# Kernel tuning notes

Hardware: AMD Instinct MI355X
Metric: run time of the kernel (lower is better)

## Reference

```python
import jax, jax.numpy as jnp
import numpy as np

NUM_BINS = 128  # 32 mid-band bins + 96 bottom-band bins
LN_EPS = 1e-5


def _mlp_scores(desc, W1, b1, g1, be1, W2, b2, Ws, bs):
    # Linear -> LayerNorm -> SiLU -> Linear -> score head
    h = desc @ W1 + b1
    mu = h.mean(-1, keepdims=True)
    var = h.var(-1, keepdims=True)
    h = (h - mu) * jax.lax.rsqrt(var + LN_EPS) * g1 + be1
    h = h * jax.nn.sigmoid(h)  # SiLU
    feat = h @ W2 + b2
    scores = (feat @ Ws + bs)[..., 0]  # [B, N]
    return scores


def _grid_ids(kpts, H, W):
    x = kpts[..., 0]
    y = kpts[..., 1]
    mid = (y > 0.2 * H) & (y <= 0.5 * H)
    btm = y > 0.5 * H
    mgx = jnp.clip((x / W * 8).astype(jnp.int32), 0, 7)
    mgy = jnp.clip(((y - 0.2 * H) / (0.3 * H) * 4).astype(jnp.int32), 0, 3)
    bgx = jnp.clip((x / W * 16).astype(jnp.int32), 0, 15)
    bgy = jnp.clip(((y - 0.5 * H) / (0.5 * H) * 6).astype(jnp.int32), 0, 5)
    gid = jnp.where(btm, 32 + bgy * 16 + bgx, jnp.where(mid, mgy * 8 + mgx, -1))
    return gid  # [B, N], -1 = not in any grid band


def _select_one(scores, gid, top_k):
    # strict-'>' loop in the original), then compact + top-k fallback.
    N = scores.shape[0]
    valid = gid >= 0
    seg = jnp.where(valid, gid, NUM_BINS)  # dump invalid pts in dummy bin
    binmax = jax.ops.segment_max(scores, seg, num_segments=NUM_BINS + 1)
    is_win = valid & (scores == binmax[seg])
    winner_idx = jax.ops.segment_min(
        jnp.where(is_win, jnp.arange(N), N), seg, num_segments=NUM_BINS + 1
    )[:NUM_BINS]  # N = empty bin sentinel
    bin_valid = winner_idx < N
    # stable sort: non-empty bins first, preserving bin order
    order = jnp.argsort((~bin_valid).astype(jnp.int32))
    winners = winner_idx[order]  # [NUM_BINS], trailing sentinels
    num_sel = jnp.sum(bin_valid)
    # mask out already-selected winners, top-k fallback on the rest
    win_mask = jnp.zeros(N, bool).at[jnp.where(bin_valid, winner_idx, N)].set(True, mode='drop')
    rem = jnp.where(win_mask, -1e10, scores)
    _, extra = jax.lax.top_k(rem, top_k)
    j = jnp.arange(top_k)
    sel = jnp.where(
        j < num_sel,
        winners[jnp.clip(j, 0, NUM_BINS - 1)],
        extra[jnp.clip(j - num_sel, 0, top_k - 1)],
    )
    return sel  # [top_k]


def setup_inputs() -> dict:
    key = jax.random.key(0)
    ks = jax.random.split(key, 4)
    B, N, IN, OUT = 8, 50000, 256, 128
    H, W = 376, 1241
    kpts = jax.random.uniform(ks[0], (B, N, 2), jnp.float32) * jnp.array([W, H], jnp.float32)
    desc = jax.random.normal(ks[1], (B, N, IN), jnp.float32)
    kw = jax.random.split(ks[2], 3)
    W1 = 0.01 * jax.random.normal(kw[0], (IN, 256), jnp.float32)
    b1 = jnp.zeros((256,), jnp.float32)
    g1 = jnp.ones((256,), jnp.float32)
    be1 = jnp.zeros((256,), jnp.float32)
    W2 = 0.01 * jax.random.normal(kw[1], (256, OUT), jnp.float32)
    b2 = jnp.zeros((OUT,), jnp.float32)
    Ws = 0.001 * jax.random.normal(kw[2], (OUT, 1), jnp.float32)
    bs = jnp.zeros((1,), jnp.float32)
    return {"kpts": kpts, "desc": desc, "H": H, "W": W, "top_k": 128,
            "W1": W1, "b1": b1, "g1": g1, "be1": be1,
            "W2": W2, "b2": b2, "Ws": Ws, "bs": bs}


def reference(kpts, desc, H, W, top_k, W1, b1, g1, be1, W2, b2, Ws, bs):
    scores = _mlp_scores(desc, W1, b1, g1, be1, W2, b2, Ws, bs)  # [B,N]
    gid = _grid_ids(kpts, H, W)  # [B,N]
    indices = jax.vmap(lambda s, g: _select_one(s, g, top_k))(scores, gid)  # [B,top_k]
    final_feat = jnp.take_along_axis(desc, indices[:, :, None], axis=1)  # [B,top_k,256]
    final_kpts = jnp.take_along_axis(kpts, indices[:, :, None], axis=1)  # [B,top_k,2]
    return final_feat, final_kpts, indices
```

## Files before the change

### kernel.cpp

```cpp
#include <hip/hip_runtime.h>

#define THREADS 256

typedef short bf16x8 __attribute__((ext_vector_type(8)));
typedef float f32x4 __attribute__((ext_vector_type(4)));

__device__ __forceinline__ unsigned short f2bf(float x) {
    unsigned u = __float_as_uint(x);
    unsigned r = u + 0x7FFFu + ((u >> 16) & 1u);
    return (unsigned short)(r >> 16);
}
__device__ __forceinline__ float bf2f(unsigned short h) {
    return __uint_as_float(((unsigned)h) << 16);
}
__device__ __forceinline__ unsigned score_key(float s) {
    unsigned u = __float_as_uint(s);
    return (u & 0x80000000u) ? ~u : (u | 0x80000000u);
}

__global__ void prep_kernel(const float* __restrict__ W2, const float* __restrict__ b2,
                            const float* __restrict__ Ws, const float* __restrict__ bs,
                            float* __restrict__ v, int OUT) {
    int j = threadIdx.x;
    float acc = 0.f;
    for (int o = 0; o < OUT; ++o) acc += W2[j * OUT + o] * Ws[o];
    v[j] = acc;
    if (j == 0) {
        float c = bs[0];
        for (int o = 0; o < OUT; ++o) c += b2[o] * Ws[o];
        v[256] = c;
    }
}

__global__ void prep_w1frag(const float* __restrict__ W1, uint4* __restrict__ wfrag) {
    const int s = blockIdx.x * 256 + threadIdx.x;
    const int rem = s & 2047;
    const int kt = s >> 11;
    const int c = rem >> 6;
    const int lane = rem & 63;
    const int h = c >> 4;
    const int nt = c & 15;
    const int col = nt * 16 + (lane & 15);
    const int kb = kt * 32 + (lane >> 4) * 8;
    unsigned pk[4];
#pragma unroll
    for (int q = 0; q < 4; ++q) {
        float x0 = W1[(size_t)(kb + 2 * q) * 256 + col];
        float x1 = W1[(size_t)(kb + 2 * q + 1) * 256 + col];
        unsigned short a0, a1;
        if (h == 0) { a0 = f2bf(x0); a1 = f2bf(x1); }
        else {
            a0 = f2bf(x0 - bf2f(f2bf(x0)));
            a1 = f2bf(x1 - bf2f(f2bf(x1)));
        }
        pk[q] = (unsigned)a0 | ((unsigned)a1 << 16);
    }
    wfrag[s] = make_uint4(pk[0], pk[1], pk[2], pk[3]);
}

__global__ void init_bins(unsigned long long* __restrict__ bins, int n) {
    int i = blockIdx.x * blockDim.x + threadIdx.x;
    if (i < n) bins[i] = 0ULL;
}

__global__ __launch_bounds__(256, 2) void score_kernel(
    const float* __restrict__ desc, const float* __restrict__ kpts,
    const uint4* __restrict__ wfrag,
    const float* __restrict__ b1, const float* __restrict__ g1, const float* __restrict__ be1,
    const int* __restrict__ Hp, const int* __restrict__ Wp,
    const float* __restrict__ v,
    float* __restrict__ scores, unsigned long long* __restrict__ bins,
    int N, int total)
{
    __shared__ uint4 AhS[8 * 64];
    __shared__ uint4 AlS[8 * 64];
    __shared__ uint4 BS[32 * 64];
    __shared__ float b1L[256], g1L[256], beL[256], vL[256];
    __shared__ float sumsL[128][2];
    __shared__ float ctermS;

    const int t = threadIdx.x;
    const int lane = t & 63;
    const int w = t >> 6;
    const int wm = w & 1, wn = w >> 1;
    const int row0 = blockIdx.x * 128;
    const int l15 = lane & 15, q4 = lane >> 4, h5 = lane >> 5;

    b1L[t] = b1[t]; g1L[t] = g1[t]; beL[t] = be1[t]; vL[t] = v[t];
    if (t == 0) ctermS = v[256];

    f32x4 acc[4][8];
#pragma unroll
    for (int m = 0; m < 4; ++m)
#pragma unroll
        for (int n = 0; n < 8; ++n) acc[m][n] = (f32x4){0.f, 0.f, 0.f, 0.f};

    const int argp = 2 * w + h5;
    const int arow = row0 + argp * 16 + l15;
    const int arowc = min(arow, total - 1);
    const int kgbit = q4 & 1;

    for (int kt = 0; kt < 8; ++kt) {
        __syncthreads();
        {
            uint4 btmp[8];
            const uint4* bsrc = wfrag + (size_t)kt * 2048 + t;
#pragma unroll
            for (int j = 0; j < 8; ++j) btmp[j] = bsrc[j * 256];
#pragma unroll
            for (int j = 0; j < 8; ++j) BS[j * 256 + t] = btmp[j];
        }
#pragma unroll
        for (int i = 0; i < 2; ++i) {
            const int kg = kgbit + 2 * i;
            const float* gp = desc + (size_t)arowc * 256 + kt * 32 + kg * 8;
            float4 f0 = *(const float4*)gp;
            float4 f1 = *(const float4*)(gp + 4);
            float f[8] = {f0.x, f0.y, f0.z, f0.w, f1.x, f1.y, f1.z, f1.w};
            unsigned hs[4], ls[4];
#pragma unroll
            for (int q = 0; q < 4; ++q) {
                unsigned short h0 = f2bf(f[2 * q]), h1 = f2bf(f[2 * q + 1]);
                unsigned short o0 = f2bf(f[2 * q] - bf2f(h0));
                unsigned short o1 = f2bf(f[2 * q + 1] - bf2f(h1));
                hs[q] = (unsigned)h0 | ((unsigned)h1 << 16);
                ls[q] = (unsigned)o0 | ((unsigned)o1 << 16);
            }
            const int slot = argp * 64 + kg * 16 + l15;
            AhS[slot] = make_uint4(hs[0], hs[1], hs[2], hs[3]);
            AlS[slot] = make_uint4(ls[0], ls[1], ls[2], ls[3]);
        }
        __syncthreads();
        bf16x8 ah[4], al[4];
#pragma unroll
        for (int m = 0; m < 4; ++m) {
            ah[m] = *(const bf16x8*)&AhS[(wm * 4 + m) * 64 + lane];
            al[m] = *(const bf16x8*)&AlS[(wm * 4 + m) * 64 + lane];
        }
#pragma unroll
        for (int n = 0; n < 8; ++n) {
            const int nt = wn * 8 + n;
            bf16x8 bh = *(const bf16x8*)&BS[nt * 64 + lane];
            bf16x8 bl = *(const bf16x8*)&BS[(16 + nt) * 64 + lane];
#pragma unroll
            for (int m = 0; m < 4; ++m) {
                acc[m][n] = __builtin_amdgcn_mfma_f32_16x16x32_bf16(ah[m], bh, acc[m][n], 0, 0, 0);
                acc[m][n] = __builtin_amdgcn_mfma_f32_16x16x32_bf16(ah[m], bl, acc[m][n], 0, 0, 0);
                acc[m][n] = __builtin_amdgcn_mfma_f32_16x16x32_bf16(al[m], bh, acc[m][n], 0, 0, 0);
                acc[m][n] = __builtin_amdgcn_mfma_f32_16x16x32_bf16(al[m], bl, acc[m][n], 0, 0, 0);
            }
        }
    }

    float bpart = 0.f;
#pragma unroll
    for (int n = 0; n < 8; ++n) bpart += b1L[wn * 128 + n * 16 + l15];

    float mu[4][4], rs[4][4];
#pragma unroll
    for (int m = 0; m < 4; ++m)
#pragma unroll
        for (int r = 0; r < 4; ++r) {
            float x = bpart;
#pragma unroll
            for (int n = 0; n < 8; ++n) x += acc[m][n][r];
#pragma unroll
            for (int mask = 1; mask <= 8; mask <<= 1) x += __shfl_xor(x, mask);
            if (l15 == 0) sumsL[wm * 64 + m * 16 + q4 * 4 + r][wn] = x;
        }
    __syncthreads();
#pragma unroll
    for (int m = 0; m < 4; ++m)
#pragma unroll
        for (int r = 0; r < 4; ++r) {
            const int rl = wm * 64 + m * 16 + q4 * 4 + r;
            mu[m][r] = (sumsL[rl][0] + sumsL[rl][1]) * (1.f / 256.f);
        }
    __syncthreads();
#pragma unroll
    for (int m = 0; m < 4; ++m)
#pragma unroll
        for (int r = 0; r < 4; ++r) {
            float x = 0.f;
#pragma unroll
            for (int n = 0; n < 8; ++n) {
                const float hv = acc[m][n][r] + b1L[wn * 128 + n * 16 + l15] - mu[m][r];
                x = fmaf(hv, hv, x);
            }
#pragma unroll
            for (int mask = 1; mask <= 8; mask <<= 1) x += __shfl_xor(x, mask);
            if (l15 == 0) sumsL[wm * 64 + m * 16 + q4 * 4 + r][wn] = x;
        }
    __syncthreads();
#pragma unroll
    for (int m = 0; m < 4; ++m)
#pragma unroll
        for (int r = 0; r < 4; ++r) {
            const int rl = wm * 64 + m * 16 + q4 * 4 + r;
            rs[m][r] = 1.f / sqrtf((sumsL[rl][0] + sumsL[rl][1]) * (1.f / 256.f) + 1e-5f);
        }
    __syncthreads();
#pragma unroll
    for (int m = 0; m < 4; ++m)
#pragma unroll
        for (int r = 0; r < 4; ++r) {
            float x = 0.f;
#pragma unroll
            for (int n = 0; n < 8; ++n) {
                const int c = wn * 128 + n * 16 + l15;
                const float hv = (acc[m][n][r] + b1L[c] - mu[m][r]) * rs[m][r] * g1L[c] + beL[c];
                const float sg = 1.f / (1.f + __expf(-hv));
                x = fmaf(vL[c], hv * sg, x);
            }
#pragma unroll
            for (int mask = 1; mask <= 8; mask <<= 1) x += __shfl_xor(x, mask);
            if (l15 == 0) sumsL[wm * 64 + m * 16 + q4 * 4 + r][wn] = x;
        }
    __syncthreads();

    if (t < 128) {
        const int row = row0 + t;
        if (row < total) {
            const float sc = sumsL[t][0] + sumsL[t][1] + ctermS;
            scores[row] = sc;
            const float Wf = (float)Wp[0];
            const int Hi = Hp[0];
            const float t02 = (float)(0.2 * (double)Hi);
            const float t05 = (float)(0.5 * (double)Hi);
            const float t03 = (float)(0.3 * (double)Hi);
            const float x = kpts[(size_t)row * 2 + 0];
            const float y = kpts[(size_t)row * 2 + 1];
            int g = -1;
            if (y > t05) {
                int bgx = (int)(x / Wf * 16.f); bgx = min(max(bgx, 0), 15);
                int bgy = (int)((y - t05) / t05 * 6.f); bgy = min(max(bgy, 0), 5);
                g = 32 + bgy * 16 + bgx;
            } else if (y > t02) {
                int mgx = (int)(x / Wf * 8.f); mgx = min(max(mgx, 0), 7);
                int mgy = (int)((y - t02) / t03 * 4.f); mgy = min(max(mgy, 0), 3);
                g = mgy * 8 + mgx;
            }
            if (g >= 0) {
                const int bb = row / N;
                const int n = row - bb * N;
                const unsigned long long pk =
                    ((unsigned long long)score_key(sc) << 32) | (unsigned)(~(unsigned)n);
                atomicMax(&bins[bb * 128 + g], pk);
            }
        }
    }
}

__global__ __launch_bounds__(256) void finalize_kernel(
    const float* __restrict__ scores, const unsigned long long* __restrict__ bins,
    const float* __restrict__ desc, const float* __restrict__ kpts,
    const int* __restrict__ tkp, float* __restrict__ out, int B, int N)
{
    const int b = blockIdx.x, t = threadIdx.x;
    const int topk = tkp[0];
    __shared__ int selL[512];
    __shared__ int nselS;
    __shared__ unsigned long long red[256];
    __shared__ unsigned long long binL[128];

    if (t < 128) binL[t] = bins[b * 128 + t];
    __syncthreads();
    if (t == 0) {
        int c = 0;
        for (int i = 0; i < 128; ++i)
            if ((binL[i] >> 32) != 0ULL) selL[c++] = (int)(~(unsigned)binL[i]);
        nselS = c;
    }
    __syncthreads();
    const int nsel = nselS;

    for (int need = nsel; need < topk; ++need) {
        unsigned long long best = 0ULL;
        for (int i = t; i < N; i += THREADS) {
            bool taken = false;
            for (int s2 = 0; s2 < need; ++s2)
                if (selL[s2] == i) { taken = true; break; }
            if (!taken) {
                const unsigned long long pk =
                    ((unsigned long long)score_key(scores[(size_t)b * N + i]) << 32)
                    | (unsigned)(~(unsigned)i);
                if (pk > best) best = pk;
            }
        }
        red[t] = best;
        __syncthreads();
        for (int off = 128; off > 0; off >>= 1) {
            if (t < off) { if (red[t + off] > red[t]) red[t] = red[t + off]; }
            __syncthreads();
        }
        if (t == 0) selL[need] = (int)(~(unsigned)red[0]);
        __syncthreads();
    }

    float* o_feat = out;
    float* o_kpts = out + (size_t)B * topk * 256;
    float* o_idx  = out + (size_t)B * topk * 258;
    for (int e = t; e < topk * 64; e += THREADS) {
        const int j = e >> 6, q4 = e & 63;
        const int n = selL[j];
        *(float4*)&o_feat[((size_t)b * topk + j) * 256 + q4 * 4] =
            *(const float4*)&desc[((size_t)b * N + n) * 256 + q4 * 4];
    }
    for (int j = t; j < topk; j += THREADS) {
        const int n = selL[j];
        o_kpts[((size_t)b * topk + j) * 2 + 0] = kpts[((size_t)b * N + n) * 2 + 0];
        o_kpts[((size_t)b * topk + j) * 2 + 1] = kpts[((size_t)b * N + n) * 2 + 1];
        o_idx[(size_t)b * topk + j] = (float)n;
    }
}

extern "C" void kernel_launch(void* const* d_in, const int* in_sizes, int n_in,
                              void* d_out, int out_size, void* d_ws, size_t ws_size,
                              hipStream_t stream) {
    const float* kpts = (const float*)d_in[0];
    const float* desc = (const float*)d_in[1];
    const int*   Hp   = (const int*)d_in[2];
    const int*   Wp   = (const int*)d_in[3];
    const int*   tkp  = (const int*)d_in[4];
    const float* W1   = (const float*)d_in[5];
    const float* b1   = (const float*)d_in[6];
    const float* g1   = (const float*)d_in[7];
    const float* be1  = (const float*)d_in[8];
    const float* W2   = (const float*)d_in[9];
    const float* b2   = (const float*)d_in[10];
    const float* Ws   = (const float*)d_in[11];
    const float* bs   = (const float*)d_in[12];

    const int total = in_sizes[1] / 256;
    const int BT    = out_size / 259;
    const int B     = BT / 128;
    const int N     = total / B;
    const int OUT   = in_sizes[11];

    float* ws_v      = (float*)d_ws;
    float* ws_scores = ws_v + 512;
    size_t off = ((size_t)(512 + total) * 4 + 255) & ~(size_t)255;
    unsigned long long* ws_bins = (unsigned long long*)((char*)d_ws + off);
    size_t off2 = (off + (size_t)B * 128 * 8 + 255) & ~(size_t)255;
    uint4* ws_wfrag = (uint4*)((char*)d_ws + off2);

    prep_kernel<<<1, 256, 0, stream>>>(W2, b2, Ws, bs, ws_v, OUT);
    prep_w1frag<<<64, 256, 0, stream>>>(W1, ws_wfrag);
    init_bins<<<(B * 128 + 255) / 256, 256, 0, stream>>>(ws_bins, B * 128);
    score_kernel<<<(total + 127) / 128, 256, 0, stream>>>(
        desc, kpts, ws_wfrag, b1, g1, be1, Hp, Wp, ws_v, ws_scores, ws_bins, N, total);
    finalize_kernel<<<B, 256, 0, stream>>>(ws_scores, ws_bins, desc, kpts, tkp,
                                           (float*)d_out, B, N);
}
```

Before: 419.9 us.

## Restructure score kernel: per-wave full rows, async double-buffered W1 tiles, single-pass LayerNorm

Each wave now owns 32 full rows across all 256 hidden columns, so A fragments are built in registers straight from global memory instead of staged through LDS. Row statistics reduce within the wave by shuffles, removing the cross-wave sumsL exchanges and their barriers. W1 fragment tiles are double-buffered in LDS with async global_load_lds copies, and the next desc chunk is prefetched while MFMAs run. LayerNorm computes mean and variance in one pass as E[x^2]-mu^2, which can lose precision, and the wider accumulator array (2x16 tiles) raises register pressure.

```diff
diff --git a/kernel.cpp b/kernel.cpp
--- a/kernel.cpp
+++ b/kernel.cpp
@@ -7,8 +7,7 @@
 
 __device__ __forceinline__ unsigned short f2bf(float x) {
     unsigned u = __float_as_uint(x);
-    unsigned r = u + 0x7FFFu + ((u >> 16) & 1u);
-    return (unsigned short)(r >> 16);
+    return (unsigned short)((u + 0x7FFFu + ((u >> 16) & 1u)) >> 16);
 }
 __device__ __forceinline__ float bf2f(unsigned short h) {
     return __uint_as_float(((unsigned)h) << 16);
@@ -16,6 +15,29 @@
 __device__ __forceinline__ unsigned score_key(float s) {
     unsigned u = __float_as_uint(s);
     return (u & 0x80000000u) ? ~u : (u | 0x80000000u);
+}
+
+__device__ __forceinline__ void split8(const float* __restrict__ f, bf16x8& hv, bf16x8& lv) {
+    union { unsigned w[4]; bf16x8 v; } H, L;
+#pragma unroll
+    for (int q = 0; q < 4; ++q) {
+        const float x0 = f[2 * q], x1 = f[2 * q + 1];
+        const unsigned b0 = __float_as_uint(x0), b1_ = __float_as_uint(x1);
+        const unsigned u0 = b0 + 0x7FFFu + ((b0 >> 16) & 1u);
+        const unsigned u1 = b1_ + 0x7FFFu + ((b1_ >> 16) & 1u);
+        const float h0 = __uint_as_float(u0 & 0xFFFF0000u);
+        const float h1 = __uint_as_float(u1 & 0xFFFF0000u);
+        const unsigned l0 = f2bf(x0 - h0), l1 = f2bf(x1 - h1);
+        H.w[q] = (u0 >> 16) | ((u1 >> 16) << 16);
+        L.w[q] = l0 | (l1 << 16);
+    }
+    hv = H.v; lv = L.v;
+}
+
+__device__ __forceinline__ void async_cp16(const uint4* g, uint4* l) {
+    __builtin_amdgcn_global_load_lds(
+        (const __attribute__((address_space(1))) unsigned int*)g,
+        (__attribute__((address_space(3))) unsigned int*)l, 16, 0, 0);
 }
 
 __global__ void prep_kernel(const float* __restrict__ W2, const float* __restrict__ b2,
@@ -72,183 +94,149 @@
     float* __restrict__ scores, unsigned long long* __restrict__ bins,
     int N, int total)
 {
-    __shared__ uint4 AhS[8 * 64];
-    __shared__ uint4 AlS[8 * 64];
-    __shared__ uint4 BS[32 * 64];
+    __shared__ uint4 BS[2][32 * 64];
     __shared__ float b1L[256], g1L[256], beL[256], vL[256];
-    __shared__ float sumsL[128][2];
-    __shared__ float ctermS;
 
     const int t = threadIdx.x;
     const int lane = t & 63;
     const int w = t >> 6;
-    const int wm = w & 1, wn = w >> 1;
-    const int row0 = blockIdx.x * 128;
-    const int l15 = lane & 15, q4 = lane >> 4, h5 = lane >> 5;
+    const int l15 = lane & 15, q4 = lane >> 4;
+    const int wrow0 = blockIdx.x * 128 + w * 32;
 
     b1L[t] = b1[t]; g1L[t] = g1[t]; beL[t] = be1[t]; vL[t] = v[t];
-    if (t == 0) ctermS = v[256];
-
-    f32x4 acc[4][8];
-#pragma unroll
-    for (int m = 0; m < 4; ++m)
-#pragma unroll
-        for (int n = 0; n < 8; ++n) acc[m][n] = (f32x4){0.f, 0.f, 0.f, 0.f};
-
-    const int argp = 2 * w + h5;
-    const int arow = row0 + argp * 16 + l15;
-    const int arowc = min(arow, total - 1);
-    const int kgbit = q4 & 1;
+
+    {
+        const uint4* bsrc = wfrag + (w * 8) * 64 + lane;
+#pragma unroll
+        for (int j = 0; j < 8; ++j)
+            async_cp16(bsrc + j * 64, &BS[0][(w * 8 + j) * 64]);
+    }
+
+    const int rA0 = min(wrow0 + l15, total - 1);
+    const int rA1 = min(wrow0 + 16 + l15, total - 1);
+    const float* pa0 = desc + (size_t)rA0 * 256 + q4 * 8;
+    const float* pa1 = desc + (size_t)rA1 * 256 + q4 * 8;
+    float4 a00 = *(const float4*)pa0, a01 = *(const float4*)(pa0 + 4);
+    float4 a10 = *(const float4*)pa1, a11 = *(const float4*)(pa1 + 4);
+
+    __syncthreads();
+
+    f32x4 acc[2][16];
+#pragma unroll
+    for (int n = 0; n < 16; ++n) {
+        const float bc = b1L[n * 16 + l15];
+        acc[0][n] = (f32x4){bc, bc, bc, bc};
+        acc[1][n] = (f32x4){bc, bc, bc, bc};
+    }
 
     for (int kt = 0; kt < 8; ++kt) {
+        const int cur = kt & 1;
+        if (kt < 7) {
+            const uint4* bsrc = wfrag + (size_t)(kt + 1) * 2048 + (w * 8) * 64 + lane;
+#pragma unroll
+            for (int j = 0; j < 8; ++j)
+                async_cp16(bsrc + j * 64, &BS[cur ^ 1][(w * 8 + j) * 64]);
+        }
+        bf16x8 ah[2], al[2];
+        {
+            float f0[8] = {a00.x, a00.y, a00.z, a00.w, a01.x, a01.y, a01.z, a01.w};
+            split8(f0, ah[0], al[0]);
+            float f1[8] = {a10.x, a10.y, a10.z, a10.w, a11.x, a11.y, a11.z, a11.w};
+            split8(f1, ah[1], al[1]);
+        }
+        if (kt < 7) {
+            const float* q0 = pa0 + (kt + 1) * 32;
+            const float* q1 = pa1 + (kt + 1) * 32;
+            a00 = *(const float4*)q0; a01 = *(const float4*)(q0 + 4);
+            a10 = *(const float4*)q1; a11 = *(const float4*)(q1 + 4);
+        }
+#pragma unroll
+        for (int g = 0; g < 4; ++g) {
+            bf16x8 bh[4], bl[4];
+#pragma unroll
+            for (int j = 0; j < 4; ++j) {
+                bh[j] = *(const bf16x8*)&BS[cur][(g * 4 + j) * 64 + lane];
+                bl[j] = *(const bf16x8*)&BS[cur][(16 + g * 4 + j) * 64 + lane];
+            }
+#pragma unroll
+            for (int p = 0; p < 4; ++p) {
+#pragma unroll
+                for (int j = 0; j < 4; ++j)
+#pragma unroll
+                    for (int m = 0; m < 2; ++m) {
+                        const bf16x8 aa = (p & 2) ? al[m] : ah[m];
+                        const bf16x8 bb = (p & 1) ? bl[j] : bh[j];
+                        acc[m][g * 4 + j] =
+                            __builtin_amdgcn_mfma_f32_16x16x32_bf16(aa, bb, acc[m][g * 4 + j], 0, 0, 0);
+                    }
+            }
+        }
         __syncthreads();
-        {
-            uint4 btmp[8];
-            const uint4* bsrc = wfrag + (size_t)kt * 2048 + t;
-#pragma unroll
-            for (int j = 0; j < 8; ++j) btmp[j] = bsrc[j * 256];
-#pragma unroll
-            for (int j = 0; j < 8; ++j) BS[j * 256 + t] = btmp[j];
-        }
-#pragma unroll
-        for (int i = 0; i < 2; ++i) {
-            const int kg = kgbit + 2 * i;
-            const float* gp = desc + (size_t)arowc * 256 + kt * 32 + kg * 8;
-            float4 f0 = *(const float4*)gp;
-            float4 f1 = *(const float4*)(gp + 4);
-            float f[8] = {f0.x, f0.y, f0.z, f0.w, f1.x, f1.y, f1.z, f1.w};
-            unsigned hs[4], ls[4];
-#pragma unroll
-            for (int q = 0; q < 4; ++q) {
-                unsigned short h0 = f2bf(f[2 * q]), h1 = f2bf(f[2 * q + 1]);
-                unsigned short o0 = f2bf(f[2 * q] - bf2f(h0));
-                unsigned short o1 = f2bf(f[2 * q + 1] - bf2f(h1));
-                hs[q] = (unsigned)h0 | ((unsigned)h1 << 16);
-                ls[q] = (unsigned)o0 | ((unsigned)o1 << 16);
-            }
-            const int slot = argp * 64 + kg * 16 + l15;
-            AhS[slot] = make_uint4(hs[0], hs[1], hs[2], hs[3]);
-            AlS[slot] = make_uint4(ls[0], ls[1], ls[2], ls[3]);
-        }
-        __syncthreads();
-        bf16x8 ah[4], al[4];
-#pragma unroll
-        for (int m = 0; m < 4; ++m) {
-            ah[m] = *(const bf16x8*)&AhS[(wm * 4 + m) * 64 + lane];
-            al[m] = *(const bf16x8*)&AlS[(wm * 4 + m) * 64 + lane];
-        }
-#pragma unroll
-        for (int n = 0; n < 8; ++n) {
-            const int nt = wn * 8 + n;
-            bf16x8 bh = *(const bf16x8*)&BS[nt * 64 + lane];
-            bf16x8 bl = *(const bf16x8*)&BS[(16 + nt) * 64 + lane];
-#pragma unroll
-            for (int m = 0; m < 4; ++m) {
-                acc[m][n] = __builtin_amdgcn_mfma_f32_16x16x32_bf16(ah[m], bh, acc[m][n], 0, 0, 0);
-                acc[m][n] = __builtin_amdgcn_mfma_f32_16x16x32_bf16(ah[m], bl, acc[m][n], 0, 0, 0);
-                acc[m][n] = __builtin_amdgcn_mfma_f32_16x16x32_bf16(al[m], bh, acc[m][n], 0, 0, 0);
-                acc[m][n] = __builtin_amdgcn_mfma_f32_16x16x32_bf16(al[m], bl, acc[m][n], 0, 0, 0);
-            }
-        }
-    }
-
-    float bpart = 0.f;
-#pragma unroll
-    for (int n = 0; n < 8; ++n) bpart += b1L[wn * 128 + n * 16 + l15];
-
-    float mu[4][4], rs[4][4];
-#pragma unroll
-    for (int m = 0; m < 4; ++m)
+    }
+
+    const float Wf = (float)Wp[0];
+    const int Hi = Hp[0];
+    const float t02 = (float)(0.2 * (double)Hi);
+    const float t05 = (float)(0.5 * (double)Hi);
+    const float t03 = (float)(0.3 * (double)Hi);
+    const float cterm = v[256];
+
+#pragma unroll
+    for (int m = 0; m < 2; ++m)
 #pragma unroll
         for (int r = 0; r < 4; ++r) {
-            float x = bpart;
-#pragma unroll
-            for (int n = 0; n < 8; ++n) x += acc[m][n][r];
-#pragma unroll
-            for (int mask = 1; mask <= 8; mask <<= 1) x += __shfl_xor(x, mask);
-            if (l15 == 0) sumsL[wm * 64 + m * 16 + q4 * 4 + r][wn] = x;
-        }
-    __syncthreads();
-#pragma unroll
-    for (int m = 0; m < 4; ++m)
-#pragma unroll
-        for (int r = 0; r < 4; ++r) {
-            const int rl = wm * 64 + m * 16 + q4 * 4 + r;
-            mu[m][r] = (sumsL[rl][0] + sumsL[rl][1]) * (1.f / 256.f);
-        }
-    __syncthreads();
-#pragma unroll
-    for (int m = 0; m < 4; ++m)
-#pragma unroll
-        for (int r = 0; r < 4; ++r) {
-            float x = 0.f;
-#pragma unroll
-            for (int n = 0; n < 8; ++n) {
-                const float hv = acc[m][n][r] + b1L[wn * 128 + n * 16 + l15] - mu[m][r];
-                x = fmaf(hv, hv, x);
-            }
-#pragma unroll
-            for (int mask = 1; mask <= 8; mask <<= 1) x += __shfl_xor(x, mask);
-            if (l15 == 0) sumsL[wm * 64 + m * 16 + q4 * 4 + r][wn] = x;
-        }
-    __syncthreads();
-#pragma unroll
-    for (int m = 0; m < 4; ++m)
-#pragma unroll
-        for (int r = 0; r < 4; ++r) {
-            const int rl = wm * 64 + m * 16 + q4 * 4 + r;
-            rs[m][r] = 1.f / sqrtf((sumsL[rl][0] + sumsL[rl][1]) * (1.f / 256.f) + 1e-5f);
-        }
-    __syncthreads();
-#pragma unroll
-    for (int m = 0; m < 4; ++m)
-#pragma unroll
-        for (int r = 0; r < 4; ++r) {
-            float x = 0.f;
-#pragma unroll
-            for (int n = 0; n < 8; ++n) {
-                const int c = wn * 128 + n * 16 + l15;
-                const float hv = (acc[m][n][r] + b1L[c] - mu[m][r]) * rs[m][r] * g1L[c] + beL[c];
+            float sx = 0.f, sq = 0.f;
+#pragma unroll
+            for (int n = 0; n < 16; ++n) {
+                const float x = acc[m][n][r];
+                sx += x; sq = fmaf(x, x, sq);
+            }
+#pragma unroll
+            for (int mask = 1; mask <= 8; mask <<= 1) {
+                sx += __shfl_xor(sx, mask);
+                sq += __shfl_xor(sq, mask);
+            }
+            const float mu = sx * (1.f / 256.f);
+            const float var = sq * (1.f / 256.f) - mu * mu;
+            const float rs = 1.f / sqrtf(var + 1e-5f);
+            float dot = 0.f;
+#pragma unroll
+            for (int n = 0; n < 16; ++n) {
+                const int c = n * 16 + l15;
+                const float hv = (acc[m][n][r] - mu) * rs * g1L[c] + beL[c];
                 const float sg = 1.f / (1.f + __expf(-hv));
-                x = fmaf(vL[c], hv * sg, x);
-            }
-#pragma unroll
-            for (int mask = 1; mask <= 8; mask <<= 1) x += __shfl_xor(x, mask);
-            if (l15 == 0) sumsL[wm * 64 + m * 16 + q4 * 4 + r][wn] = x;
-        }
-    __syncthreads();
-
-    if (t < 128) {
-        const int row = row0 + t;
-        if (row < total) {
-            const float sc = sumsL[t][0] + sumsL[t][1] + ctermS;
-            scores[row] = sc;
-            const float Wf = (float)Wp[0];
-            const int Hi = Hp[0];
-            const float t02 = (float)(0.2 * (double)Hi);
-            const float t05 = (float)(0.5 * (double)Hi);
-            const float t03 = (float)(0.3 * (double)Hi);
-            const float x = kpts[(size_t)row * 2 + 0];
-            const float y = kpts[(size_t)row * 2 + 1];
-            int g = -1;
-            if (y > t05) {
-                int bgx = (int)(x / Wf * 16.f); bgx = min(max(bgx, 0), 15);
-                int bgy = (int)((y - t05) / t05 * 6.f); bgy = min(max(bgy, 0), 5);
-                g = 32 + bgy * 16 + bgx;
-            } else if (y > t02) {
-                int mgx = (int)(x / Wf * 8.f); mgx = min(max(mgx, 0), 7);
-                int mgy = (int)((y - t02) / t03 * 4.f); mgy = min(max(mgy, 0), 3);
-                g = mgy * 8 + mgx;
-            }
-            if (g >= 0) {
-                const int bb = row / N;
-                const int n = row - bb * N;
-                const unsigned long long pk =
-                    ((unsigned long long)score_key(sc) << 32) | (unsigned)(~(unsigned)n);
-                atomicMax(&bins[bb * 128 + g], pk);
-            }
-        }
-    }
+                dot = fmaf(vL[c], hv * sg, dot);
+            }
+#pragma unroll
+            for (int mask = 1; mask <= 8; mask <<= 1) dot += __shfl_xor(dot, mask);
+
+            if (l15 == 0) {
+                const int row = wrow0 + m * 16 + q4 * 4 + r;
+                if (row < total) {
+                    const float sc = dot + cterm;
+                    scores[row] = sc;
+                    const float x = kpts[(size_t)row * 2 + 0];
+                    const float y = kpts[(size_t)row * 2 + 1];
+                    int g = -1;
+                    if (y > t05) {
+                        int bgx = (int)(x / Wf * 16.f); bgx = min(max(bgx, 0), 15);
+                        int bgy = (int)((y - t05) / t05 * 6.f); bgy = min(max(bgy, 0), 5);
+                        g = 32 + bgy * 16 + bgx;
+                    } else if (y > t02) {
+                        int mgx = (int)(x / Wf * 8.f); mgx = min(max(mgx, 0), 7);
+                        int mgy = (int)((y - t02) / t03 * 4.f); mgy = min(max(mgy, 0), 3);
+                        g = mgy * 8 + mgx;
+                    }
+                    if (g >= 0) {
+                        const int bb = row / N;
+                        const int n = row - bb * N;
+                        const unsigned long long pk =
+                            ((unsigned long long)score_key(sc) << 32) | (unsigned)(~(unsigned)n);
+                        atomicMax(&bins[bb * 128 + g], pk);
+                    }
+                }
+            }
+        }
 }
 
 __global__ __launch_bounds__(256) void finalize_kernel(
```

Result: slower. 430.4 us (+2.5%).
